# Performance work log

Measured on AMD Instinct MI355X. Metric: run time of the kernel, lower is better.

The kernel has to match this reference:

```python
import jax, jax.numpy as jnp
import numpy as np

OUT_H, OUT_W = 6, 6
SPATIAL_SCALE = 1.0
SAMPLING_RATIO = 2  # fixed grid (Mask R-CNN standard); aligned=True semantics below


def setup_inputs() -> dict:
    key = jax.random.key(0)
    k1, k2, k3 = jax.random.split(key, 3)
    B, C, H, W = 8, 256, 128, 128
    N = 64
    x = jax.random.normal(k1, (B, C, H, W), dtype=jnp.float32)
    # boxes in (x1, y1, x2, y2) image coords, guaranteed x1<x2, y1<y2
    xs = jnp.sort(jax.random.uniform(k2, (B, N, 2), dtype=jnp.float32) * W, axis=-1)
    ys = jnp.sort(jax.random.uniform(k3, (B, N, 2), dtype=jnp.float32) * H, axis=-1)
    boxes = jnp.stack([xs[..., 0], ys[..., 0], xs[..., 1], ys[..., 1]], axis=-1)
    return {"x": x, "boxes": boxes}


def _interp_1d(coords, size):
    # torchvision bilinear_interpolate semantics along one axis
    valid = (coords >= -1.0) & (coords <= size)
    c = jnp.maximum(coords, 0.0)
    low0 = jnp.floor(c).astype(jnp.int32)
    at_edge = low0 >= size - 1
    low = jnp.where(at_edge, size - 1, low0)
    high = jnp.where(at_edge, size - 1, low0 + 1)
    frac = jnp.where(at_edge, 0.0, c - low0.astype(c.dtype))
    w_lo = jnp.where(valid, 1.0 - frac, 0.0)
    w_hi = jnp.where(valid, frac, 0.0)
    return low, high, w_lo, w_hi


def _roi_align_one(feat, boxes):
    # feat: [C, H, W], boxes: [N, 4] -> [N, C, OUT_H, OUT_W]
    C, H, W = feat.shape
    gh, gw = SAMPLING_RATIO, SAMPLING_RATIO
    x1 = boxes[:, 0] * SPATIAL_SCALE - 0.5  # aligned=True half-pixel offset
    y1 = boxes[:, 1] * SPATIAL_SCALE - 0.5
    x2 = boxes[:, 2] * SPATIAL_SCALE - 0.5
    y2 = boxes[:, 3] * SPATIAL_SCALE - 0.5
    bin_h = (y2 - y1) / OUT_H  # [N]
    bin_w = (x2 - x1) / OUT_W
    # sample positions in bin units: pos[k] for k = bin_idx*g + i -> bin_idx + (i+0.5)/g
    pos_y = (jnp.arange(OUT_H, dtype=jnp.float32)[:, None]
             + (jnp.arange(gh, dtype=jnp.float32)[None, :] + 0.5) / gh).reshape(-1)
    pos_x = (jnp.arange(OUT_W, dtype=jnp.float32)[:, None]
             + (jnp.arange(gw, dtype=jnp.float32)[None, :] + 0.5) / gw).reshape(-1)
    ys = y1[:, None] + pos_y[None, :] * bin_h[:, None]  # [N, OUT_H*gh]
    xs = x1[:, None] + pos_x[None, :] * bin_w[:, None]  # [N, OUT_W*gw]
    yl, yh, wy0, wy1 = _interp_1d(ys, H)
    xl, xh, wx0, wx1 = _interp_1d(xs, W)
    flat = feat.reshape(C, H * W)

    def g(yi, xi):
        idx = yi[:, :, None] * W + xi[:, None, :]  # [N, Yg, Xg]
        return flat[:, idx]                        # [C, N, Yg, Xg]

    val = (wy0[:, :, None] * wx0[:, None, :] * g(yl, xl)
           + wy0[:, :, None] * wx1[:, None, :] * g(yl, xh)
           + wy1[:, :, None] * wx0[:, None, :] * g(yh, xl)
           + wy1[:, :, None] * wx1[:, None, :] * g(yh, xh))
    N = boxes.shape[0]
    # average the gh*gw samples within each output bin (count = gh*gw)
    val = val.reshape(C, N, OUT_H, gh, OUT_W, gw).mean(axis=(3, 5))
    return jnp.transpose(val, (1, 0, 2, 3))  # [N, C, OUT_H, OUT_W]


def reference(x, boxes):
    # x: [B, C, H, W], boxes: [B, N, 4] -> [B, N, C, OUT_H, OUT_W]
    return jax.vmap(_roi_align_one)(x, boxes)
```

## Files before the change

### kernel.cpp

```cpp
#include <hip/hip_runtime.h>

#define B 8
#define C 256
#define H 128
#define W 128
#define HW (H * W)
#define NBOX 64
#define OUT_H 6
#define OUT_W 6
#define NBINS (OUT_H * OUT_W)
#define ENT_PER_BOX 24
#define TBL_PER_B (NBOX * ENT_PER_BOX)
#define PITCH 132
#define PLANE_ELEMS ((H + 1) * PITCH)
#define NOUT (NBOX * NBINS)
#define PLANES_PER_BLOCK 4
#define NTHREADS 512
#define NBLK (B * C / PLANES_PER_BLOCK)
#define TAIL (NOUT - 4 * NTHREADS)

using f4 = float __attribute__((ext_vector_type(4)));

__device__ __forceinline__ void interp1d(float coord, int size,
                                         int& lo, float& w0) {
    bool valid = (coord >= -1.0f) && (coord <= (float)size);
    float c = fmaxf(coord, 0.0f);
    int low0 = (int)floorf(c);
    bool at_edge = (low0 >= size - 1);
    lo = at_edge ? (size - 1) : low0;
    float frac = at_edge ? 0.0f : (c - (float)low0);
    w0 = valid ? (1.0f - frac) : 0.0f;
}

__global__ __launch_bounds__(NTHREADS, 4)
void roi_persist_kernel(const float* __restrict__ x,
                        const float* __restrict__ boxes,
                        float* __restrict__ out) {
    __shared__ float buf[PLANE_ELEMS];
    __shared__ float2 stab[TBL_PER_B];

    const int blk = blockIdx.x;
    const int b = blk >> 6;
    const int c0 = (blk & 63) * PLANES_PER_BLOCK;
    const int tid = threadIdx.x;

    f4 r0, r1, r2, r3, r4, r5, r6, r7;
    {
        const f4* src = (const f4*)(x + (size_t)(b * C + c0) * HW);
        r0 = __builtin_nontemporal_load(&src[0 * NTHREADS + tid]);
        r1 = __builtin_nontemporal_load(&src[1 * NTHREADS + tid]);
        r2 = __builtin_nontemporal_load(&src[2 * NTHREADS + tid]);
        r3 = __builtin_nontemporal_load(&src[3 * NTHREADS + tid]);
        r4 = __builtin_nontemporal_load(&src[4 * NTHREADS + tid]);
        r5 = __builtin_nontemporal_load(&src[5 * NTHREADS + tid]);
        r6 = __builtin_nontemporal_load(&src[6 * NTHREADS + tid]);
        r7 = __builtin_nontemporal_load(&src[7 * NTHREADS + tid]);
    }

    #pragma unroll
    for (int i = tid; i < TBL_PER_B; i += NTHREADS) {
        const int n = i / ENT_PER_BOX;
        const int k = i - n * ENT_PER_BOX;
        const float* bx = boxes + ((size_t)(b * NBOX + n)) * 4;
        const float x1 = bx[0] - 0.5f;
        const float y1 = bx[1] - 0.5f;
        const float x2 = bx[2] - 0.5f;
        const float y2 = bx[3] - 0.5f;
        const int kk = (k < 12) ? k : (k - 12);
        const float pos = (float)(kk >> 1) + ((float)(kk & 1) + 0.5f) * 0.5f;
        float coord;
        if (k < 12) coord = y1 + pos * ((y2 - y1) * (1.0f / OUT_H));
        else        coord = x1 + pos * ((x2 - x1) * (1.0f / OUT_W));
        int lo; float w0;
        interp1d(coord, 128, lo, w0);
        if (k < 12) stab[i] = make_float2(0.25f * w0, __int_as_float(lo * PITCH));
        else        stab[i] = make_float2(w0,         __int_as_float(lo));
    }

    {
        const f4 z4 = {0.f, 0.f, 0.f, 0.f};
        if (tid < H + 1) {
            *(f4*)&buf[tid * PITCH + W] = z4;
        } else if (tid < H + 1 + 32) {
            *(f4*)&buf[H * PITCH + (tid - (H + 1)) * 4] = z4;
        }
    }

    #pragma unroll
    for (int i = 0; i < 8; ++i) {
        const int m = i * NTHREADS + tid;
        const f4 v = (i == 0) ? r0 : (i == 1) ? r1 : (i == 2) ? r2
                   : (i == 3) ? r3 : (i == 4) ? r4 : (i == 5) ? r5
                   : (i == 6) ? r6 : r7;
        *(f4*)&buf[(m >> 5) * PITCH + ((m & 31) << 2)] = v;
    }
    __syncthreads();

    float hwy0[5], hwy2[5], hwx0[5], hwx2[5];
    int   ha00[5], ha01[5], ha20[5], ha21[5];
    int   hofs[5];
    #pragma unroll
    for (int o = 0; o < 5; ++o) {
        int k = o * NTHREADS + tid;
        if (o == 4 && tid >= TAIL) k = NOUT - 1;
        const int n = (k * 3641) >> 17;
        const int bin = k - n * NBINS;
        const int oh = (bin * 43) >> 8;
        const int ow = bin - oh * OUT_W;
        const float2* e = stab + n * ENT_PER_BOX;
        const float2 ey0 = e[oh * 2 + 0];
        const float2 ey1 = e[oh * 2 + 1];
        const float2 ex0 = e[12 + ow * 2 + 0];
        const float2 ex1 = e[12 + ow * 2 + 1];
        const int ry0 = __float_as_int(ey0.y);
        const int ry1 = __float_as_int(ey1.y);
        const int cx0 = __float_as_int(ex0.y);
        const int cx1 = __float_as_int(ex1.y);
        hwy0[o] = ey0.x;  hwy2[o] = ey1.x;
        hwx0[o] = ex0.x;  hwx2[o] = ex1.x;
        ha00[o] = ry0 + cx0;
        ha01[o] = ry0 + cx1;
        ha20[o] = ry1 + cx0;
        ha21[o] = ry1 + cx1;
        hofs[o] = n * (C * NBINS) + bin;
    }

    #pragma unroll 1
    for (int p = 0; p < PLANES_PER_BLOCK; ++p) {
        if (p < PLANES_PER_BLOCK - 1) {
            const f4* src = (const f4*)(x + (size_t)(b * C + c0 + p + 1) * HW);
            r0 = __builtin_nontemporal_load(&src[0 * NTHREADS + tid]);
            r1 = __builtin_nontemporal_load(&src[1 * NTHREADS + tid]);
            r2 = __builtin_nontemporal_load(&src[2 * NTHREADS + tid]);
            r3 = __builtin_nontemporal_load(&src[3 * NTHREADS + tid]);
            r4 = __builtin_nontemporal_load(&src[4 * NTHREADS + tid]);
            r5 = __builtin_nontemporal_load(&src[5 * NTHREADS + tid]);
            r6 = __builtin_nontemporal_load(&src[6 * NTHREADS + tid]);
            r7 = __builtin_nontemporal_load(&src[7 * NTHREADS + tid]);
        }

        float* ob = out + ((size_t)(b * NBOX) * C + c0 + p) * NBINS;
        #pragma unroll
        for (int o = 0; o < 5; ++o) {
            const float wy0 = hwy0[o], wy1 = 0.25f - wy0;
            const float wy2 = hwy2[o], wy3 = 0.25f - wy2;
            const float wx0 = hwx0[o], wx1 = 1.0f - wx0;
            const float wx2 = hwx2[o], wx3 = 1.0f - wx2;
            const float* p00 = buf + ha00[o];
            const float* p01 = buf + ha01[o];
            const float* p20 = buf + ha20[o];
            const float* p21 = buf + ha21[o];

            const float h00 = wx0 * p00[0]     + wx1 * p00[1];
            const float h10 = wx0 * p00[PITCH] + wx1 * p00[PITCH + 1];
            const float h01 = wx2 * p01[0]     + wx3 * p01[1];
            const float h11 = wx2 * p01[PITCH] + wx3 * p01[PITCH + 1];
            const float h20 = wx0 * p20[0]     + wx1 * p20[1];
            const float h30 = wx0 * p20[PITCH] + wx1 * p20[PITCH + 1];
            const float h21 = wx2 * p21[0]     + wx3 * p21[1];
            const float h31 = wx2 * p21[PITCH] + wx3 * p21[PITCH + 1];

            const float acc = wy0 * (h00 + h01) + wy1 * (h10 + h11)
                            + wy2 * (h20 + h21) + wy3 * (h30 + h31);
            if (o < 4 || tid < TAIL)
                __builtin_nontemporal_store(acc, &ob[hofs[o]]);
        }

        if (p < PLANES_PER_BLOCK - 1) {
            __syncthreads();
            #pragma unroll
            for (int i = 0; i < 8; ++i) {
                const int m = i * NTHREADS + tid;
                const f4 v = (i == 0) ? r0 : (i == 1) ? r1 : (i == 2) ? r2
                           : (i == 3) ? r3 : (i == 4) ? r4 : (i == 5) ? r5
                           : (i == 6) ? r6 : r7;
                *(f4*)&buf[(m >> 5) * PITCH + ((m & 31) << 2)] = v;
            }
            __syncthreads();
        }
    }
}

extern "C" void kernel_launch(void* const* d_in, const int* in_sizes, int n_in,
                              void* d_out, int out_size, void* d_ws, size_t ws_size,
                              hipStream_t stream) {
    const float* x     = (const float*)d_in[0];
    const float* boxes = (const float*)d_in[1];
    float* out = (float*)d_out;

    roi_persist_kernel<<<NBLK, NTHREADS, 0, stream>>>(x, boxes, out);
}
```

Baseline: 194.0 us.

## Interleave channel pairs in shared memory and double threads per block

Each block now processes eight channels as four interleaved pairs, storing two planes per shared-memory cell as float2 so every bilinear gather fetches both channels with one 8-byte load. The block grows to 1024 threads, which cuts each thread's outputs per pass from 5 to 3, and the grid is halved. The aim is to amortise LDS gather addressing and index work over two channels. In exchange shared memory per block doubles to about 146KB, which limits blocks per CU, and register pressure may rise under the larger block.

```diff
diff --git a/kernel.cpp b/kernel.cpp
--- a/kernel.cpp
+++ b/kernel.cpp
@@ -12,14 +12,16 @@
 #define ENT_PER_BOX 24
 #define TBL_PER_B (NBOX * ENT_PER_BOX)
 #define PITCH 132
-#define PLANE_ELEMS ((H + 1) * PITCH)
+#define PAIR_CELLS ((H + 1) * PITCH)
 #define NOUT (NBOX * NBINS)
-#define PLANES_PER_BLOCK 4
-#define NTHREADS 512
-#define NBLK (B * C / PLANES_PER_BLOCK)
-#define TAIL (NOUT - 4 * NTHREADS)
+#define PAIRS_PER_BLOCK 4
+#define CPB (2 * PAIRS_PER_BLOCK)
+#define NTHREADS 1024
+#define NBLK (B * C / CPB)
+#define TAIL (NOUT - 2 * NTHREADS)
 
 using f4 = float __attribute__((ext_vector_type(4)));
+using f2 = float __attribute__((ext_vector_type(2)));
 
 __device__ __forceinline__ void interp1d(float coord, int size,
                                          int& lo, float& w0) {
@@ -36,28 +38,28 @@
 void roi_persist_kernel(const float* __restrict__ x,
                         const float* __restrict__ boxes,
                         float* __restrict__ out) {
-    __shared__ float buf[PLANE_ELEMS];
-    __shared__ float2 stab[TBL_PER_B];
+    __shared__ f2 buf2[PAIR_CELLS];
+    __shared__ f2 stab[TBL_PER_B];
 
     const int blk = blockIdx.x;
-    const int b = blk >> 6;
-    const int c0 = (blk & 63) * PLANES_PER_BLOCK;
+    const int b = blk >> 5;
+    const int c0 = (blk & 31) * CPB;
     const int tid = threadIdx.x;
 
-    f4 r0, r1, r2, r3, r4, r5, r6, r7;
+    f4 a0, a1, a2, a3, b0, b1, b2, b3;
     {
-        const f4* src = (const f4*)(x + (size_t)(b * C + c0) * HW);
-        r0 = __builtin_nontemporal_load(&src[0 * NTHREADS + tid]);
-        r1 = __builtin_nontemporal_load(&src[1 * NTHREADS + tid]);
-        r2 = __builtin_nontemporal_load(&src[2 * NTHREADS + tid]);
-        r3 = __builtin_nontemporal_load(&src[3 * NTHREADS + tid]);
-        r4 = __builtin_nontemporal_load(&src[4 * NTHREADS + tid]);
-        r5 = __builtin_nontemporal_load(&src[5 * NTHREADS + tid]);
-        r6 = __builtin_nontemporal_load(&src[6 * NTHREADS + tid]);
-        r7 = __builtin_nontemporal_load(&src[7 * NTHREADS + tid]);
-    }
-
-    #pragma unroll
+        const f4* sa = (const f4*)(x + (size_t)(b * C + c0 + 0) * HW);
+        const f4* sb = (const f4*)(x + (size_t)(b * C + c0 + 1) * HW);
+        a0 = __builtin_nontemporal_load(&sa[0 * NTHREADS + tid]);
+        a1 = __builtin_nontemporal_load(&sa[1 * NTHREADS + tid]);
+        a2 = __builtin_nontemporal_load(&sa[2 * NTHREADS + tid]);
+        a3 = __builtin_nontemporal_load(&sa[3 * NTHREADS + tid]);
+        b0 = __builtin_nontemporal_load(&sb[0 * NTHREADS + tid]);
+        b1 = __builtin_nontemporal_load(&sb[1 * NTHREADS + tid]);
+        b2 = __builtin_nontemporal_load(&sb[2 * NTHREADS + tid]);
+        b3 = __builtin_nontemporal_load(&sb[3 * NTHREADS + tid]);
+    }
+
     for (int i = tid; i < TBL_PER_B; i += NTHREADS) {
         const int n = i / ENT_PER_BOX;
         const int k = i - n * ENT_PER_BOX;
@@ -73,45 +75,47 @@
         else        coord = x1 + pos * ((x2 - x1) * (1.0f / OUT_W));
         int lo; float w0;
         interp1d(coord, 128, lo, w0);
-        if (k < 12) stab[i] = make_float2(0.25f * w0, __int_as_float(lo * PITCH));
-        else        stab[i] = make_float2(w0,         __int_as_float(lo));
+        if (k < 12) stab[i] = (f2){0.25f * w0, __int_as_float(lo * PITCH)};
+        else        stab[i] = (f2){w0,         __int_as_float(lo)};
     }
 
     {
         const f4 z4 = {0.f, 0.f, 0.f, 0.f};
         if (tid < H + 1) {
-            *(f4*)&buf[tid * PITCH + W] = z4;
-        } else if (tid < H + 1 + 32) {
-            *(f4*)&buf[H * PITCH + (tid - (H + 1)) * 4] = z4;
+            *(f4*)&buf2[tid * PITCH + 128] = z4;
+            *(f4*)&buf2[tid * PITCH + 130] = z4;
+        } else if (tid >= 200 && tid < 266) {
+            *(f4*)&buf2[H * PITCH + (tid - 200) * 2] = z4;
         }
     }
 
     #pragma unroll
-    for (int i = 0; i < 8; ++i) {
+    for (int i = 0; i < 4; ++i) {
         const int m = i * NTHREADS + tid;
-        const f4 v = (i == 0) ? r0 : (i == 1) ? r1 : (i == 2) ? r2
-                   : (i == 3) ? r3 : (i == 4) ? r4 : (i == 5) ? r5
-                   : (i == 6) ? r6 : r7;
-        *(f4*)&buf[(m >> 5) * PITCH + ((m & 31) << 2)] = v;
+        const f4 a = (i == 0) ? a0 : (i == 1) ? a1 : (i == 2) ? a2 : a3;
+        const f4 v = (i == 0) ? b0 : (i == 1) ? b1 : (i == 2) ? b2 : b3;
+        const int cell = (m >> 5) * PITCH + ((m & 31) << 2);
+        *(f4*)&buf2[cell]     = (f4){a.x, v.x, a.y, v.y};
+        *(f4*)&buf2[cell + 2] = (f4){a.z, v.z, a.w, v.w};
     }
     __syncthreads();
 
-    float hwy0[5], hwy2[5], hwx0[5], hwx2[5];
-    int   ha00[5], ha01[5], ha20[5], ha21[5];
-    int   hofs[5];
+    float hwy0[3], hwy2[3], hwx0[3], hwx2[3];
+    int   ha00[3], ha01[3], ha20[3], ha21[3];
+    int   hofs[3];
     #pragma unroll
-    for (int o = 0; o < 5; ++o) {
+    for (int o = 0; o < 3; ++o) {
         int k = o * NTHREADS + tid;
-        if (o == 4 && tid >= TAIL) k = NOUT - 1;
+        if (o == 2 && tid >= TAIL) k = NOUT - 1;
         const int n = (k * 3641) >> 17;
         const int bin = k - n * NBINS;
         const int oh = (bin * 43) >> 8;
         const int ow = bin - oh * OUT_W;
-        const float2* e = stab + n * ENT_PER_BOX;
-        const float2 ey0 = e[oh * 2 + 0];
-        const float2 ey1 = e[oh * 2 + 1];
-        const float2 ex0 = e[12 + ow * 2 + 0];
-        const float2 ex1 = e[12 + ow * 2 + 1];
+        const f2* e = stab + n * ENT_PER_BOX;
+        const f2 ey0 = e[oh * 2 + 0];
+        const f2 ey1 = e[oh * 2 + 1];
+        const f2 ex0 = e[12 + ow * 2 + 0];
+        const f2 ex1 = e[12 + ow * 2 + 1];
         const int ry0 = __float_as_int(ey0.y);
         const int ry1 = __float_as_int(ey1.y);
         const int cx0 = __float_as_int(ex0.y);
@@ -126,55 +130,78 @@
     }
 
     #pragma unroll 1
-    for (int p = 0; p < PLANES_PER_BLOCK; ++p) {
-        if (p < PLANES_PER_BLOCK - 1) {
-            const f4* src = (const f4*)(x + (size_t)(b * C + c0 + p + 1) * HW);
-            r0 = __builtin_nontemporal_load(&src[0 * NTHREADS + tid]);
-            r1 = __builtin_nontemporal_load(&src[1 * NTHREADS + tid]);
-            r2 = __builtin_nontemporal_load(&src[2 * NTHREADS + tid]);
-            r3 = __builtin_nontemporal_load(&src[3 * NTHREADS + tid]);
-            r4 = __builtin_nontemporal_load(&src[4 * NTHREADS + tid]);
-            r5 = __builtin_nontemporal_load(&src[5 * NTHREADS + tid]);
-            r6 = __builtin_nontemporal_load(&src[6 * NTHREADS + tid]);
-            r7 = __builtin_nontemporal_load(&src[7 * NTHREADS + tid]);
-        }
-
-        float* ob = out + ((size_t)(b * NBOX) * C + c0 + p) * NBINS;
+    for (int pp = 0; pp < PAIRS_PER_BLOCK; ++pp) {
+        if (pp < PAIRS_PER_BLOCK - 1) {
+            const f4* sa = (const f4*)(x + (size_t)(b * C + c0 + 2 * pp + 2) * HW);
+            const f4* sb = (const f4*)(x + (size_t)(b * C + c0 + 2 * pp + 3) * HW);
+            a0 = __builtin_nontemporal_load(&sa[0 * NTHREADS + tid]);
+            a1 = __builtin_nontemporal_load(&sa[1 * NTHREADS + tid]);
+            a2 = __builtin_nontemporal_load(&sa[2 * NTHREADS + tid]);
+            a3 = __builtin_nontemporal_load(&sa[3 * NTHREADS + tid]);
+            b0 = __builtin_nontemporal_load(&sb[0 * NTHREADS + tid]);
+            b1 = __builtin_nontemporal_load(&sb[1 * NTHREADS + tid]);
+            b2 = __builtin_nontemporal_load(&sb[2 * NTHREADS + tid]);
+            b3 = __builtin_nontemporal_load(&sb[3 * NTHREADS + tid]);
+        }
+
+        float* ob = out + ((size_t)(b * NBOX) * C + c0 + 2 * pp) * NBINS;
         #pragma unroll
-        for (int o = 0; o < 5; ++o) {
+        for (int o = 0; o < 3; ++o) {
             const float wy0 = hwy0[o], wy1 = 0.25f - wy0;
             const float wy2 = hwy2[o], wy3 = 0.25f - wy2;
             const float wx0 = hwx0[o], wx1 = 1.0f - wx0;
             const float wx2 = hwx2[o], wx3 = 1.0f - wx2;
-            const float* p00 = buf + ha00[o];
-            const float* p01 = buf + ha01[o];
-            const float* p20 = buf + ha20[o];
-            const float* p21 = buf + ha21[o];
-
-            const float h00 = wx0 * p00[0]     + wx1 * p00[1];
-            const float h10 = wx0 * p00[PITCH] + wx1 * p00[PITCH + 1];
-            const float h01 = wx2 * p01[0]     + wx3 * p01[1];
-            const float h11 = wx2 * p01[PITCH] + wx3 * p01[PITCH + 1];
-            const float h20 = wx0 * p20[0]     + wx1 * p20[1];
-            const float h30 = wx0 * p20[PITCH] + wx1 * p20[PITCH + 1];
-            const float h21 = wx2 * p21[0]     + wx3 * p21[1];
-            const float h31 = wx2 * p21[PITCH] + wx3 * p21[PITCH + 1];
-
-            const float acc = wy0 * (h00 + h01) + wy1 * (h10 + h11)
-                            + wy2 * (h20 + h21) + wy3 * (h30 + h31);
-            if (o < 4 || tid < TAIL)
-                __builtin_nontemporal_store(acc, &ob[hofs[o]]);
-        }
-
-        if (p < PLANES_PER_BLOCK - 1) {
+            const f2* q00 = buf2 + ha00[o];
+            const f2* q01 = buf2 + ha01[o];
+            const f2* q20 = buf2 + ha20[o];
+            const f2* q21 = buf2 + ha21[o];
+
+            const f2 v00a = q00[0], v00b = q00[1];
+            const f2 v00c = q00[PITCH], v00d = q00[PITCH + 1];
+            const f2 v01a = q01[0], v01b = q01[1];
+            const f2 v01c = q01[PITCH], v01d = q01[PITCH + 1];
+            const f2 v20a = q20[0], v20b = q20[1];
+            const f2 v20c = q20[PITCH], v20d = q20[PITCH + 1];
+            const f2 v21a = q21[0], v21b = q21[1];
+            const f2 v21c = q21[PITCH], v21d = q21[PITCH + 1];
+
+            const float h00A = wx0 * v00a.x + wx1 * v00b.x;
+            const float h10A = wx0 * v00c.x + wx1 * v00d.x;
+            const float h01A = wx2 * v01a.x + wx3 * v01b.x;
+            const float h11A = wx2 * v01c.x + wx3 * v01d.x;
+            const float h20A = wx0 * v20a.x + wx1 * v20b.x;
+            const float h30A = wx0 * v20c.x + wx1 * v20d.x;
+            const float h21A = wx2 * v21a.x + wx3 * v21b.x;
+            const float h31A = wx2 * v21c.x + wx3 * v21d.x;
+            const float accA = wy0 * (h00A + h01A) + wy1 * (h10A + h11A)
+                             + wy2 * (h20A + h21A) + wy3 * (h30A + h31A);
+            const float h00B = wx0 * v00a.y + wx1 * v00b.y;
+            const float h10B = wx0 * v00c.y + wx1 * v00d.y;
+            const float h01B = wx2 * v01a.y + wx3 * v01b.y;
+            const float h11B = wx2 * v01c.y + wx3 * v01d.y;
+            const float h20B = wx0 * v20a.y + wx1 * v20b.y;
+            const float h30B = wx0 * v20c.y + wx1 * v20d.y;
+            const float h21B = wx2 * v21a.y + wx3 * v21b.y;
+            const float h31B = wx2 * v21c.y + wx3 * v21d.y;
+            const float accB = wy0 * (h00B + h01B) + wy1 * (h10B + h11B)
+                             + wy2 * (h20B + h21B) + wy3 * (h30B + h31B);
+
+            if (o < 2 || tid < TAIL) {
+                __builtin_nontemporal_store(accA, &ob[hofs[o]]);
+                __builtin_nontemporal_store(accB, &ob[hofs[o] + NBINS]);
+            }
+        }
+
+        if (pp < PAIRS_PER_BLOCK - 1) {
             __syncthreads();
             #pragma unroll
-            for (int i = 0; i < 8; ++i) {
+            for (int i = 0; i < 4; ++i) {
                 const int m = i * NTHREADS + tid;
-                const f4 v = (i == 0) ? r0 : (i == 1) ? r1 : (i == 2) ? r2
-                           : (i == 3) ? r3 : (i == 4) ? r4 : (i == 5) ? r5
-                           : (i == 6) ? r6 : r7;
-                *(f4*)&buf[(m >> 5) * PITCH + ((m & 31) << 2)] = v;
+                const f4 a = (i == 0) ? a0 : (i == 1) ? a1 : (i == 2) ? a2 : a3;
+                const f4 v = (i == 0) ? b0 : (i == 1) ? b1 : (i == 2) ? b2 : b3;
+                const int cell = (m >> 5) * PITCH + ((m & 31) << 2);
+                *(f4*)&buf2[cell]     = (f4){a.x, v.x, a.y, v.y};
+                *(f4*)&buf2[cell + 2] = (f4){a.z, v.z, a.w, v.w};
             }
             __syncthreads();
         }
```

After: 194.0 us. No clear change (-0.0%).

## Double-buffer feature planes in LDS via direct global-to-LDS DMA loads

Applied to the files above, without the earlier changes.

Replaces the register-staged plane loads (global to VGPR, then LDS stores) with __builtin_amdgcn_global_load_lds, which copies each feature plane straight into LDS. Two LDS buffers let the next plane stream in while the current one is sampled, and this removes one of the two barriers per plane. The block grows to 1024 threads handling 8 planes, and the padded pitch is dropped to match the DMA layout. In exchange, LDS use rises to roughly 144 KB, so only one block fits per CU, and correctness now depends on the barrier waiting for the async LDS writes to finish.

```diff
diff --git a/kernel.cpp b/kernel.cpp
--- a/kernel.cpp
+++ b/kernel.cpp
@@ -1,4 +1,5 @@
 #include <hip/hip_runtime.h>
+#include <stdint.h>
 
 #define B 8
 #define C 256
@@ -11,15 +12,17 @@
 #define NBINS (OUT_H * OUT_W)
 #define ENT_PER_BOX 24
 #define TBL_PER_B (NBOX * ENT_PER_BOX)
-#define PITCH 132
-#define PLANE_ELEMS ((H + 1) * PITCH)
+#define PITCH 128
+#define PLANE_DW ((H + 1) * PITCH)
 #define NOUT (NBOX * NBINS)
-#define PLANES_PER_BLOCK 4
-#define NTHREADS 512
+#define PLANES_PER_BLOCK 8
+#define NTHREADS 1024
 #define NBLK (B * C / PLANES_PER_BLOCK)
-#define TAIL (NOUT - 4 * NTHREADS)
+#define TAIL (NOUT - 2 * NTHREADS)
 
 using f4 = float __attribute__((ext_vector_type(4)));
+typedef const __attribute__((address_space(1))) uint32_t gu32;
+typedef __attribute__((address_space(3))) uint32_t lu32;
 
 __device__ __forceinline__ void interp1d(float coord, int size,
                                          int& lo, float& w0) {
@@ -32,32 +35,35 @@
     w0 = valid ? (1.0f - frac) : 0.0f;
 }
 
+__device__ __forceinline__ void dma_plane(const float* __restrict__ gsrc,
+                                          float* ldst, int tid) {
+    const int w = tid >> 6;
+    const int lane = tid & 63;
+    #pragma unroll
+    for (int i = 0; i < 4; ++i) {
+        const int chunk = (w * 4 + i) * 1024;
+        __builtin_amdgcn_global_load_lds(
+            (gu32*)((const char*)gsrc + chunk + lane * 16),
+            (lu32*)((char*)ldst + chunk),
+            16, 0, 0);
+    }
+}
+
 __global__ __launch_bounds__(NTHREADS, 4)
 void roi_persist_kernel(const float* __restrict__ x,
                         const float* __restrict__ boxes,
                         float* __restrict__ out) {
-    __shared__ float buf[PLANE_ELEMS];
+    __shared__ float buf0[PLANE_DW];
+    __shared__ float buf1[PLANE_DW];
     __shared__ float2 stab[TBL_PER_B];
 
     const int blk = blockIdx.x;
-    const int b = blk >> 6;
-    const int c0 = (blk & 63) * PLANES_PER_BLOCK;
+    const int b = blk >> 5;
+    const int c0 = (blk & 31) * PLANES_PER_BLOCK;
     const int tid = threadIdx.x;
 
-    f4 r0, r1, r2, r3, r4, r5, r6, r7;
-    {
-        const f4* src = (const f4*)(x + (size_t)(b * C + c0) * HW);
-        r0 = __builtin_nontemporal_load(&src[0 * NTHREADS + tid]);
-        r1 = __builtin_nontemporal_load(&src[1 * NTHREADS + tid]);
-        r2 = __builtin_nontemporal_load(&src[2 * NTHREADS + tid]);
-        r3 = __builtin_nontemporal_load(&src[3 * NTHREADS + tid]);
-        r4 = __builtin_nontemporal_load(&src[4 * NTHREADS + tid]);
-        r5 = __builtin_nontemporal_load(&src[5 * NTHREADS + tid]);
-        r6 = __builtin_nontemporal_load(&src[6 * NTHREADS + tid]);
-        r7 = __builtin_nontemporal_load(&src[7 * NTHREADS + tid]);
-    }
+    dma_plane(x + (size_t)(b * C + c0) * HW, buf0, tid);
 
-    #pragma unroll
     for (int i = tid; i < TBL_PER_B; i += NTHREADS) {
         const int n = i / ENT_PER_BOX;
         const int k = i - n * ENT_PER_BOX;
@@ -79,30 +85,23 @@
 
     {
         const f4 z4 = {0.f, 0.f, 0.f, 0.f};
-        if (tid < H + 1) {
-            *(f4*)&buf[tid * PITCH + W] = z4;
-        } else if (tid < H + 1 + 32) {
-            *(f4*)&buf[H * PITCH + (tid - (H + 1)) * 4] = z4;
+        if (tid < 32) {
+            *(f4*)&buf0[H * PITCH + tid * 4] = z4;
+        } else if (tid < 64) {
+            *(f4*)&buf1[H * PITCH + (tid - 32) * 4] = z4;
+        } else if (tid == 64) {
+            buf1[0] = 0.0f;
         }
-    }
-
-    #pragma unroll
-    for (int i = 0; i < 8; ++i) {
-        const int m = i * NTHREADS + tid;
-        const f4 v = (i == 0) ? r0 : (i == 1) ? r1 : (i == 2) ? r2
-                   : (i == 3) ? r3 : (i == 4) ? r4 : (i == 5) ? r5
-                   : (i == 6) ? r6 : r7;
-        *(f4*)&buf[(m >> 5) * PITCH + ((m & 31) << 2)] = v;
     }
     __syncthreads();
 
-    float hwy0[5], hwy2[5], hwx0[5], hwx2[5];
-    int   ha00[5], ha01[5], ha20[5], ha21[5];
-    int   hofs[5];
+    float hwy0[3], hwy2[3], hwx0[3], hwx2[3];
+    int   ha00[3], ha01[3], ha20[3], ha21[3];
+    int   hofs[3];
     #pragma unroll
-    for (int o = 0; o < 5; ++o) {
+    for (int o = 0; o < 3; ++o) {
         int k = o * NTHREADS + tid;
-        if (o == 4 && tid >= TAIL) k = NOUT - 1;
+        if (o == 2 && tid >= TAIL) k = NOUT - 1;
         const int n = (k * 3641) >> 17;
         const int bin = k - n * NBINS;
         const int oh = (bin * 43) >> 8;
@@ -127,29 +126,23 @@
 
     #pragma unroll 1
     for (int p = 0; p < PLANES_PER_BLOCK; ++p) {
-        if (p < PLANES_PER_BLOCK - 1) {
-            const f4* src = (const f4*)(x + (size_t)(b * C + c0 + p + 1) * HW);
-            r0 = __builtin_nontemporal_load(&src[0 * NTHREADS + tid]);
-            r1 = __builtin_nontemporal_load(&src[1 * NTHREADS + tid]);
-            r2 = __builtin_nontemporal_load(&src[2 * NTHREADS + tid]);
-            r3 = __builtin_nontemporal_load(&src[3 * NTHREADS + tid]);
-            r4 = __builtin_nontemporal_load(&src[4 * NTHREADS + tid]);
-            r5 = __builtin_nontemporal_load(&src[5 * NTHREADS + tid]);
-            r6 = __builtin_nontemporal_load(&src[6 * NTHREADS + tid]);
-            r7 = __builtin_nontemporal_load(&src[7 * NTHREADS + tid]);
-        }
+        float* cur = (p & 1) ? buf1 : buf0;
+        float* nxt = (p & 1) ? buf0 : buf1;
+
+        if (p < PLANES_PER_BLOCK - 1)
+            dma_plane(x + (size_t)(b * C + c0 + p + 1) * HW, nxt, tid);
 
         float* ob = out + ((size_t)(b * NBOX) * C + c0 + p) * NBINS;
         #pragma unroll
-        for (int o = 0; o < 5; ++o) {
+        for (int o = 0; o < 3; ++o) {
             const float wy0 = hwy0[o], wy1 = 0.25f - wy0;
             const float wy2 = hwy2[o], wy3 = 0.25f - wy2;
             const float wx0 = hwx0[o], wx1 = 1.0f - wx0;
             const float wx2 = hwx2[o], wx3 = 1.0f - wx2;
-            const float* p00 = buf + ha00[o];
-            const float* p01 = buf + ha01[o];
-            const float* p20 = buf + ha20[o];
-            const float* p21 = buf + ha21[o];
+            const float* p00 = cur + ha00[o];
+            const float* p01 = cur + ha01[o];
+            const float* p20 = cur + ha20[o];
+            const float* p21 = cur + ha21[o];
 
             const float h00 = wx0 * p00[0]     + wx1 * p00[1];
             const float h10 = wx0 * p00[PITCH] + wx1 * p00[PITCH + 1];
@@ -162,22 +155,12 @@
 
             const float acc = wy0 * (h00 + h01) + wy1 * (h10 + h11)
                             + wy2 * (h20 + h21) + wy3 * (h30 + h31);
-            if (o < 4 || tid < TAIL)
+            if (o < 2 || tid < TAIL)
                 __builtin_nontemporal_store(acc, &ob[hofs[o]]);
         }
 
-        if (p < PLANES_PER_BLOCK - 1) {
+        if (p < PLANES_PER_BLOCK - 1)
             __syncthreads();
-            #pragma unroll
-            for (int i = 0; i < 8; ++i) {
-                const int m = i * NTHREADS + tid;
-                const f4 v = (i == 0) ? r0 : (i == 1) ? r1 : (i == 2) ? r2
-                           : (i == 3) ? r3 : (i == 4) ? r4 : (i == 5) ? r5
-                           : (i == 6) ? r6 : r7;
-                *(f4*)&buf[(m >> 5) * PITCH + ((m & 31) << 2)] = v;
-            }
-            __syncthreads();
-        }
     }
 }
 
```

Result: slower. 209.4 us (+7.9%).
